# Optimization experiments

Measured on AMD Instinct MI355X. Metric: run time of the kernel, lower is better.

The kernel has to match this reference:

```python
import jax, jax.numpy as jnp
import numpy as np
from jax import lax

B, S, D, H, HFF, T = 256, 33, 42, 128, 256, 20
BN_EPS = 1e-5

def _bn(x, g, b):
    # eval-mode BatchNorm1d with running_mean=0, running_var=1
    return x * (g / jnp.sqrt(1.0 + BN_EPS)) + b

def _gelu(x):
    return jax.nn.gelu(x, approximate=False)  # torch default GELU (exact)

def setup_inputs() -> dict:
    key = jax.random.key(0)
    ks = iter(jax.random.split(key, 48))
    w = lambda shp, s=0.02: jax.random.normal(next(ks), shp, dtype=jnp.float32) * s
    z = lambda shp: jnp.zeros(shp, jnp.float32)
    o = lambda shp: jnp.ones(shp, jnp.float32)
    inp = {
        'interaction_path': jax.random.normal(next(ks), (B, S, D), dtype=jnp.float32),
        'timestamps': jnp.broadcast_to(jnp.arange(S, dtype=jnp.float32) * 0.1, (B, S)),
        # initial encoder: Linear(42->128), BN, GELU, Linear(128->128), BN
        'enc_w1': w((D, H)), 'enc_b1': z(H), 'enc_g1': o(H), 'enc_be1': z(H),
        'enc_w2': w((H, H)), 'enc_b2': z(H), 'enc_g2': o(H), 'enc_be2': z(H),
        # vector field: 128->256 (BN,GELU), 256->256 (BN,GELU) x2, 256->5376
        'vf_w0': w((H, HFF)), 'vf_b0': z(HFF), 'vf_g0': o(HFF), 'vf_be0': z(HFF),
        'vf_w1': w((HFF, HFF)), 'vf_b1': z(HFF), 'vf_g1': o(HFF), 'vf_be1': z(HFF),
        'vf_w2': w((HFF, HFF)), 'vf_b2': z(HFF), 'vf_g2': o(HFF), 'vf_be2': z(HFF),
        'vf_w3': w((HFF, H * D)), 'vf_b3': z(H * D),
        # multihead attention (seq_len = 1 -> softmax is identically 1)
        'wv': w((H, H)), 'bv': z(H), 'wo': w((H, H)), 'bo': z(H),
        # 20 trait decoders, stacked: 128->64->32->1
        'dw1': w((T, H, 64)), 'db1': z((T, 64)),
        'dw2': w((T, 64, 32)), 'db2': z((T, 32)),
        'dw3': w((T, 32, 1)), 'db3': z((T, 1)),
    }
    return inp

def reference(interaction_path, timestamps,
              enc_w1, enc_b1, enc_g1, enc_be1, enc_w2, enc_b2, enc_g2, enc_be2,
              vf_w0, vf_b0, vf_g0, vf_be0, vf_w1, vf_b1, vf_g1, vf_be1,
              vf_w2, vf_b2, vf_g2, vf_be2, vf_w3, vf_b3,
              wv, bv, wo, bo,
              dw1, db1, dw2, db2, dw3, db3):
    b = interaction_path.shape[0]
    # ---- initial encoder on X[:, 0] ----
    x0 = interaction_path[:, 0]                      # [B, D]
    h = _gelu(_bn(x0 @ enc_w1 + enc_b1, enc_g1, enc_be1))
    z0 = _bn(h @ enc_w2 + enc_b2, enc_g2, enc_be2)   # [B, H]

    # ---- CDE vector field: z -> [B, H, D] ----
    def vf(zz):
        y = _gelu(_bn(zz @ vf_w0 + vf_b0, vf_g0, vf_be0))
        y = _gelu(_bn(y @ vf_w1 + vf_b1, vf_g1, vf_be1))
        y = _gelu(_bn(y @ vf_w2 + vf_b2, vf_g2, vf_be2))
        return (y @ vf_w3 + vf_b3).reshape(b, H, D)

    def g(zz, dxdt):  # f(z) @ dX/dt  -> [B, H]
        return jnp.einsum('bhd,bd->bh', vf(zz), dxdt)

    # linear-interpolation control path: piecewise-constant derivative
    t = timestamps[0]                                # [S]
    dt = t[1:] - t[:-1]                              # [S-1]
    dX = interaction_path[:, 1:] - interaction_path[:, :-1]   # [B, S-1, D]
    dXdt = dX / dt[None, :, None]                    # [B, S-1, D]

    def step(zz, x):
        dxdt, hstep = x
        k1 = g(zz, dxdt)
        k2 = g(zz + 0.5 * hstep * k1, dxdt)
        k3 = g(zz + 0.5 * hstep * k2, dxdt)
        k4 = g(zz + hstep * k3, dxdt)
        return zz + (hstep / 6.0) * (k1 + 2.0 * k2 + 2.0 * k3 + k4), None

    zT, _ = lax.scan(step, z0, (jnp.swapaxes(dXdt, 0, 1), dt))  # [B, H]

    # ---- self-attention over a length-1 sequence: softmax==1 -> out_proj(v) ----
    attended = (zT @ wv + bv) @ wo + bo              # [B, H]

    # ---- 20 trait decoders (stacked / vectorized) ----
    h1 = _gelu(jnp.einsum('bh,thd->tbd', attended, dw1) + db1[:, None, :])
    h2 = _gelu(jnp.einsum('tbd,tde->tbe', h1, dw2) + db2[:, None, :])
    out = jax.nn.sigmoid(jnp.einsum('tbe,teo->tbo', h2, dw3) + db3[:, None, :])
    return jnp.transpose(out[..., 0], (1, 0))        # [B, 20]
```

## Files before the change

### kernel.cpp

```cpp
#include <hip/hip_runtime.h>
#include <cstdint>

constexpr int B    = 256;
constexpr int S    = 33;
constexpr int D    = 42;
constexpr int H    = 128;
constexpr int HFF  = 256;
constexpr int T    = 20;
constexpr int NSTEP = S - 1;
constexpr int DP   = D / 2;
constexpr int ADW  = 8192;
constexpr int CH   = 16;
constexpr int NCH  = NSTEP / CH;
#define BN_SCALE 0.9999950000374997f

typedef _Float16 h2v __attribute__((ext_vector_type(2)));
typedef _Float16 f16x8 __attribute__((ext_vector_type(8)));
typedef float    f32x4 __attribute__((ext_vector_type(4)));
union UH2 { uint32_t u; h2v h; };

__device__ __forceinline__ float fdot2u(uint32_t a, uint32_t b, float c) {
    UH2 x, y; x.u = a; y.u = b;
    return __builtin_amdgcn_fdot2(x.h, y.h, c, false);
}
__device__ __forceinline__ uint32_t packh2(float a, float b) {
    UH2 u; u.h = h2v{(_Float16)a, (_Float16)b}; return u.u;
}
__device__ __forceinline__ float gelu_exact(float x) {
    return 0.5f * x * (1.0f + erff(x * 0.70710678118654752f));
}
__device__ __forceinline__ float gelu_fast(float x) {
    float inner = x * (1.0f + 0.044715f * x * x);
    float E = __expf(1.5957691216f * inner);
    return x * E * __frcp_rn(E + 1.0f);
}
__device__ __forceinline__ int aswz(int idx) {
    return (idx & ~31) | ((idx & 31) ^ (((idx >> 9) & 3) << 1));
}

__global__ void pack_kernel(const float* __restrict__ w0, const float* __restrict__ w1,
                            const float* __restrict__ w2, const float* __restrict__ w3,
                            uint32_t* __restrict__ wcol, uint32_t* __restrict__ wp) {
    int idx = blockIdx.x * 256 + threadIdx.x;
    if (idx < 160 * 512) {
        int r = idx >> 9, t = idx & 511;
        int j = t >> 1, half = t & 1;
        float a, bb;
        if (r < 32)      { int ip = half * 32 + r;      a = w0[(2*ip)*HFF + j]; bb = w0[(2*ip+1)*HFF + j]; }
        else if (r < 96) { int ip = half * 64 + (r-32); a = w1[(2*ip)*HFF + j]; bb = w1[(2*ip+1)*HFF + j]; }
        else             { int ip = half * 64 + (r-96); a = w2[(2*ip)*HFF + j]; bb = w2[(2*ip+1)*HFF + j]; }
        wcol[idx] = packh2(a, bb);
    }
    if (idx < 32768 * 32) {
        int m = idx >> 5, dd = (idx & 31) * 2;
        int e = 4 * (m >> 9) + (m & 3);
        int h = (m >> 2) & 127;
        const float* row = w3 + (size_t)e * (H * D) + h * D;
        float a = (dd     < D) ? row[dd]     : 0.f;
        float b = (dd + 1 < D) ? row[dd + 1] : 0.f;
        wp[idx] = packh2(a, b);
    }
}

__global__ void prep_kernel(const float* __restrict__ path, const float* __restrict__ ts,
                            const float* __restrict__ ew1, const float* __restrict__ eb1,
                            const float* __restrict__ eg1, const float* __restrict__ ebe1,
                            const float* __restrict__ ew2, const float* __restrict__ eb2,
                            const float* __restrict__ eg2, const float* __restrict__ ebe2,
                            const float* __restrict__ b3,
                            float* __restrict__ zbuf, uint32_t* __restrict__ dxp,
                            float* __restrict__ bd3g, float* __restrict__ dtb) {
    __shared__ float x0[D], hb[H], dxs[NSTEP][D];
    int b = blockIdx.x, tid = threadIdx.x;
    if (tid < D) x0[tid] = path[b * S * D + tid];
    __syncthreads();
    {
        float acc = eb1[tid];
        for (int d = 0; d < D; ++d) acc += x0[d] * ew1[d * H + tid];
        hb[tid] = gelu_exact(acc * (eg1[tid] * BN_SCALE) + ebe1[tid]);
    }
    __syncthreads();
    {
        float acc = eb2[tid];
        for (int i = 0; i < H; ++i) acc += hb[i] * ew2[i * H + tid];
        zbuf[b * H + tid] = acc * (eg2[tid] * BN_SCALE) + ebe2[tid];
    }
    for (int idx = tid; idx < NSTEP * 32; idx += 128) {
        int s = idx >> 5, j2 = idx & 31;
        uint32_t val = 0;
        if (j2 < DP) {
            float dtv = ts[s + 1] - ts[s];
            int base = b * S * D + s * D + 2 * j2;
            float v0 = (path[base + D] - path[base]) / dtv;
            float v1 = (path[base + D + 1] - path[base + 1]) / dtv;
            dxs[s][2 * j2] = v0; dxs[s][2 * j2 + 1] = v1;
            val = packh2(v0, v1);
        }
        dxp[((size_t)(s * B + b)) * 32 + j2] = val;
    }
    __syncthreads();
    for (int s = 0; s < NSTEP; ++s) {
        float a = 0.f;
        for (int d = 0; d < D; ++d) a += b3[tid * D + d] * dxs[s][d];
        bd3g[(size_t)(s * B + b) * H + tid] = a;
    }
    if (b == 0 && tid < NSTEP) dtb[tid] = ts[tid + 1] - ts[tid];
}

__global__ void __launch_bounds__(256) amm_kernel(
    const uint32_t* __restrict__ wp, const uint32_t* __restrict__ dxp,
    uint32_t* __restrict__ Ach, int s0) {
    int t = threadIdx.x;
    int l = t & 63, wid = t >> 6;
    int mg = (blockIdx.x & 63) * 4 + wid;
    int sg = blockIdx.x >> 6;
    int lr = l & 15, lk = l >> 4;
    const char* wpB = (const char*)wp;
    const char* dxB = (const char*)dxp + (size_t)s0 * B * 128;
    char* asB = (char*)Ach;
    f16x8 af0[8], af1[8];
#pragma unroll
    for (int mi = 0; mi < 8; ++mi) {
        const f16x8* p = (const f16x8*)(wpB + ((size_t)(mg * 8 + mi) * 16 + lr) * 128 + lk * 16);
        af0[mi] = p[0]; af1[mi] = p[4];
    }
#pragma unroll
    for (int si = 0; si < 8; ++si) {
        int q = sg * 128 + si * 16 + lr;
        const f16x8* bp = (const f16x8*)(dxB + (size_t)q * 128 + lk * 16);
        f16x8 b0 = bp[0], b1 = bp[4];
        char* outB = asB + (size_t)q * 32768 + (mg * 128 + lk * 4);
#pragma unroll
        for (int mi = 0; mi < 8; ++mi) {
            f32x4 acc = {0.f, 0.f, 0.f, 0.f};
            acc = __builtin_amdgcn_mfma_f32_16x16x32_f16(af0[mi], b0, acc, 0, 0, 0);
            acc = __builtin_amdgcn_mfma_f32_16x16x32_f16(af1[mi], b1, acc, 0, 0, 0);
            uint32_t P0 = packh2(acc[0], acc[1]) + 0x00800080u;
            uint32_t P1 = packh2(acc[2], acc[3]) + 0x00800080u;
            uint32_t Q = __builtin_amdgcn_perm(P1, P0, 0x07050301u);
            *(uint32_t*)(outB + mi * 16) = Q;
        }
    }
}

__global__ void __launch_bounds__(512, 1)
__attribute__((amdgpu_waves_per_eu(2, 8)))
scan_kernel(
    const uint32_t* __restrict__ wcol, const uint32_t* __restrict__ Ach,
    const float* __restrict__ vb0, const float* __restrict__ vg0, const float* __restrict__ vbe0,
    const float* __restrict__ vb1, const float* __restrict__ vg1, const float* __restrict__ vbe1,
    const float* __restrict__ vb2, const float* __restrict__ vg2, const float* __restrict__ vbe2,
    const float* __restrict__ bd3g, const float* __restrict__ dtb,
    float* __restrict__ zbuf, int s0) {
    __shared__ __align__(16) uint32_t ABUF[2][ADW];
    __shared__ __align__(16) uint32_t zzPd[72];
    __shared__ __align__(16) uint32_t yA[136], yB[136], yC[136];
    int t = threadIdx.x, b = blockIdx.x;
    int j = t >> 1, half = t & 1;
    int h = t >> 2, g = t & 3;
    int hswz = h ^ (g << 3);
    uint32_t w0h[32], w1h[64], w2h[64];
#pragma unroll
    for (int r = 0; r < 32; ++r) w0h[r] = wcol[r * 512 + t];
#pragma unroll
    for (int r = 0; r < 64; ++r) w1h[r] = wcol[(32 + r) * 512 + t];
#pragma unroll
    for (int r = 0; r < 64; ++r) w2h[r] = wcol[(96 + r) * 512 + t];
    float c0s = vg0[j] * BN_SCALE, c0o = vb0[j] * c0s + vbe0[j];
    float c1s = vg1[j] * BN_SCALE, c1o = vb1[j] * c1s + vbe1[j];
    float c2s = vg2[j] * BN_SCALE, c2o = vb2[j] * c2s + vbe2[j];
    float zf = zbuf[b * H + h];
    {
        const uint4* Ag = (const uint4*)(Ach + (size_t)b * ADW);
        uint4 a0 = Ag[t], a1 = Ag[512 + t], a2 = Ag[1024 + t], a3 = Ag[1536 + t];
        uint4* Ad = (uint4*)ABUF[0];
        Ad[aswz(t)] = a0; Ad[aswz(512 + t)] = a1;
        Ad[aswz(1024 + t)] = a2; Ad[aswz(1536 + t)] = a3;
    }
    {
        float zhi = __shfl_down(zf, 4, 64);
        if ((t & 7) == 0) {
            int ip = t >> 3;
            zzPd[(ip >> 5) * 36 + (ip & 31)] = packh2(zf, zhi);
        }
    }
    __syncthreads();

    for (int sl = 0; sl < CH; ++sl) {
        int s = s0 + sl;
        float hstep = dtb[s];
        float bd3 = bd3g[(size_t)(s * B + b) * H + h];
        uint4 pf0, pf1, pf2, pf3;
        {
            int sn = (sl + 1 < CH) ? sl + 1 : sl;
            const uint4* Ag = (const uint4*)(Ach + (size_t)(sn * B + b) * ADW);
            pf0 = Ag[t]; pf1 = Ag[512 + t]; pf2 = Ag[1024 + t]; pf3 = Ag[1536 + t];
        }
        const uint32_t* AL = ABUF[sl & 1];
        float ksum = 0.f, kcur = 0.f;
        for (int r = 0; r < 4; ++r) {
            {
                float pa = 0.f, pb = 0.f, pc = 0.f, pd = 0.f;
                const uint4* zq = (const uint4*)(zzPd + half * 36);
#pragma unroll
                for (int u4 = 0; u4 < 8; ++u4) {
                    uint4 zv = zq[u4];
                    pa = fdot2u(w0h[4*u4+0], zv.x, pa); pb = fdot2u(w0h[4*u4+1], zv.y, pb);
                    pc = fdot2u(w0h[4*u4+2], zv.z, pc); pd = fdot2u(w0h[4*u4+3], zv.w, pd);
                }
                float p = (pa + pb) + (pc + pd);
                p += __shfl_xor(p, 1, 64);
                float v = gelu_fast(p * c0s + c0o);
                float vhi = __shfl_down(v, 2, 64);
                if ((t & 3) == 0) {
                    int ip = t >> 2;
                    yA[(ip >> 6) * 68 + (ip & 63)] = packh2(v, vhi);
                }
            }
            __syncthreads();
            {
                float pa = 0.f, pb = 0.f, pc = 0.f, pd = 0.f;
                const uint4* yq = (const uint4*)(yA + half * 68);
#pragma unroll
                for (int u4 = 0; u4 < 16; ++u4) {
                    uint4 yv = yq[u4];
                    pa = fdot2u(w1h[4*u4+0], yv.x, pa); pb = fdot2u(w1h[4*u4+1], yv.y, pb);
                    pc = fdot2u(w1h[4*u4+2], yv.z, pc); pd = fdot2u(w1h[4*u4+3], yv.w, pd);
                }
                float p = (pa + pb) + (pc + pd);
                p += __shfl_xor(p, 1, 64);
                float v = gelu_fast(p * c1s + c1o);
                float vhi = __shfl_down(v, 2, 64);
                if ((t & 3) == 0) {
                    int ip = t >> 2;
                    yB[(ip >> 6) * 68 + (ip & 63)] = packh2(v, vhi);
                }
            }
            __syncthreads();
            {
                float pa = 0.f, pb = 0.f, pc = 0.f, pd = 0.f;
                const uint4* yq = (const uint4*)(yB + half * 68);
#pragma unroll
                for (int u4 = 0; u4 < 16; ++u4) {
                    uint4 yv = yq[u4];
                    pa = fdot2u(w2h[4*u4+0], yv.x, pa); pb = fdot2u(w2h[4*u4+1], yv.y, pb);
                    pc = fdot2u(w2h[4*u4+2], yv.z, pc); pd = fdot2u(w2h[4*u4+3], yv.w, pd);
                }
                float p = (pa + pb) + (pc + pd);
                p += __shfl_xor(p, 1, 64);
                float v = gelu_fast(p * c2s + c2o);
                float vhi = __shfl_down(v, 2, 64);
                if ((t & 3) == 0) {
                    int ip = t >> 2;
                    yC[(ip >> 6) * 68 + (ip & 63)] = packh2(v, vhi);
                }
            }
            __syncthreads();
            {
                float pA = 0.f, pB = 0.f, pC = 0.f, pD = 0.f;
                int ybase = (g >> 1) * 68 + (g & 1) * 32;
                const uint4* yq = (const uint4*)(yC + ybase);
#pragma unroll
                for (int kk = 0; kk < 8; ++kk) {
                    uint4 yv = yq[kk];
                    int k0 = g * 16 + 2 * kk;
                    uint32_t Qa = AL[k0 * 128 + hswz];
                    uint32_t Qb = AL[(k0 + 1) * 128 + hswz];
                    pA = fdot2u(__builtin_amdgcn_perm(0u, Qa, 0x010C000Cu), yv.x, pA);
                    pB = fdot2u(__builtin_amdgcn_perm(0u, Qa, 0x030C020Cu), yv.y, pB);
                    pC = fdot2u(__builtin_amdgcn_perm(0u, Qb, 0x010C000Cu), yv.z, pC);
                    pD = fdot2u(__builtin_amdgcn_perm(0u, Qb, 0x030C020Cu), yv.w, pD);
                }
                float ptot = (pA + pB) + (pC + pD);
                ptot += __shfl_xor(ptot, 1, 64);
                ptot += __shfl_xor(ptot, 2, 64);
                kcur = bd3 + ptot;
                float wsm = (r == 1 || r == 2) ? 2.f : 1.f;
                ksum += wsm * kcur;
                float zz;
                if (r < 3) {
                    float cin = (r == 2) ? 1.f : 0.5f;
                    zz = zf + cin * hstep * kcur;
                } else {
                    zf += hstep * (1.f / 6.f) * ksum;
                    zz = zf;
                }
                float zhi = __shfl_down(zz, 4, 64);
                if ((t & 7) == 0) {
                    int ip = t >> 3;
                    zzPd[(ip >> 5) * 36 + (ip & 31)] = packh2(zz, zhi);
                }
            }
            if (r == 3) {
                uint4* Ad = (uint4*)ABUF[(sl + 1) & 1];
                Ad[aswz(t)] = pf0; Ad[aswz(512 + t)] = pf1;
                Ad[aswz(1024 + t)] = pf2; Ad[aswz(1536 + t)] = pf3;
            }
            __syncthreads();
        }
    }
    if ((t & 3) == 0) zbuf[b * H + h] = zf;
}

__global__ void att_kernel(const float* __restrict__ zbuf,
                           const float* __restrict__ wv, const float* __restrict__ bv,
                           const float* __restrict__ wo, const float* __restrict__ bo,
                           float* __restrict__ att) {
    __shared__ float zl[H], v[H];
    int b = blockIdx.x, tid = threadIdx.x;
    zl[tid] = zbuf[b * H + tid];
    __syncthreads();
    {
        float acc = bv[tid];
#pragma unroll 8
        for (int i = 0; i < H; ++i) acc += zl[i] * wv[i * H + tid];
        v[tid] = acc;
    }
    __syncthreads();
    {
        float acc = bo[tid];
#pragma unroll 8
        for (int i = 0; i < H; ++i) acc += v[i] * wo[i * H + tid];
        att[b * H + tid] = acc;
    }
}

__global__ void __launch_bounds__(64) dec_kernel(
    const float* __restrict__ att,
    const float* __restrict__ dw1, const float* __restrict__ db1,
    const float* __restrict__ dw2, const float* __restrict__ db2,
    const float* __restrict__ dw3, const float* __restrict__ db3,
    float* __restrict__ out) {
    int bid = blockIdx.x;
    int t = bid >> 8, b = bid & 255;
    int tid = threadIdx.x;
    __shared__ float al[H], h1l[64];
    al[tid] = att[b * H + tid];
    al[tid + 64] = att[b * H + tid + 64];
    __syncthreads();
    {
        float acc = db1[t * 64 + tid];
#pragma unroll 8
        for (int i = 0; i < H; ++i) acc += al[i] * dw1[t * H * 64 + i * 64 + tid];
        h1l[tid] = gelu_exact(acc);
    }
    __syncthreads();
    float v = 0.f;
    if (tid < 32) {
        float acc = db2[t * 32 + tid];
#pragma unroll 8
        for (int i = 0; i < 64; ++i) acc += h1l[i] * dw2[t * 64 * 32 + i * 32 + tid];
        v = gelu_exact(acc) * dw3[t * 32 + tid];
    }
#pragma unroll
    for (int off = 16; off >= 1; off >>= 1) v += __shfl_down(v, off, 64);
    if (tid == 0) out[b * T + t] = 1.f / (1.f + expf(-(v + db3[t])));
}

extern "C" void kernel_launch(void* const* d_in, const int* in_sizes, int n_in,
                              void* d_out, int out_size, void* d_ws, size_t ws_size,
                              hipStream_t stream) {
    const float* path = (const float*)d_in[0];
    const float* ts   = (const float*)d_in[1];
    const float* ew1  = (const float*)d_in[2];
    const float* eb1  = (const float*)d_in[3];
    const float* eg1  = (const float*)d_in[4];
    const float* ebe1 = (const float*)d_in[5];
    const float* ew2  = (const float*)d_in[6];
    const float* eb2  = (const float*)d_in[7];
    const float* eg2  = (const float*)d_in[8];
    const float* ebe2 = (const float*)d_in[9];
    const float* vw0  = (const float*)d_in[10];
    const float* vb0  = (const float*)d_in[11];
    const float* vg0  = (const float*)d_in[12];
    const float* vbe0 = (const float*)d_in[13];
    const float* vw1  = (const float*)d_in[14];
    const float* vb1  = (const float*)d_in[15];
    const float* vg1  = (const float*)d_in[16];
    const float* vbe1 = (const float*)d_in[17];
    const float* vw2  = (const float*)d_in[18];
    const float* vb2  = (const float*)d_in[19];
    const float* vg2  = (const float*)d_in[20];
    const float* vbe2 = (const float*)d_in[21];
    const float* vw3  = (const float*)d_in[22];
    const float* vb3  = (const float*)d_in[23];
    const float* wv   = (const float*)d_in[24];
    const float* bv   = (const float*)d_in[25];
    const float* wo   = (const float*)d_in[26];
    const float* bo   = (const float*)d_in[27];
    const float* dw1  = (const float*)d_in[28];
    const float* db1  = (const float*)d_in[29];
    const float* dw2  = (const float*)d_in[30];
    const float* db2  = (const float*)d_in[31];
    const float* dw3  = (const float*)d_in[32];
    const float* db3  = (const float*)d_in[33];

    char* ws = (char*)d_ws;
    size_t off = 0;
    auto take = [&](size_t bytes) { char* p = ws + off; off += (bytes + 255) & ~(size_t)255; return p; };
    uint32_t* Ach   = (uint32_t*)take((size_t)CH * B * ADW * 4);
    uint32_t* dxp   = (uint32_t*)take((size_t)NSTEP * B * 32 * 4);
    float*    bd3g  = (float*)take((size_t)NSTEP * B * H * 4);
    float*    dtb   = (float*)take(NSTEP * 4);
    float*    zbuf  = (float*)take((size_t)B * H * 4);
    float*    att   = (float*)take((size_t)B * H * 4);
    uint32_t* wcol  = (uint32_t*)take((size_t)160 * 512 * 4);
    uint32_t* wp    = (uint32_t*)take((size_t)32768 * 32 * 4);

    pack_kernel<<<(32768 * 32 + 255) / 256, 256, 0, stream>>>(vw0, vw1, vw2, vw3, wcol, wp);
    prep_kernel<<<B, 128, 0, stream>>>(path, ts, ew1, eb1, eg1, ebe1,
                                       ew2, eb2, eg2, ebe2, vb3, zbuf, dxp, bd3g, dtb);
    for (int c = 0; c < NCH; ++c) {
        amm_kernel<<<2048, 256, 0, stream>>>(wp, dxp, Ach, c * CH);
        scan_kernel<<<B, 512, 0, stream>>>(wcol, Ach,
                                           vb0, vg0, vbe0, vb1, vg1, vbe1, vb2, vg2, vbe2,
                                           bd3g, dtb, zbuf, c * CH);
    }
    att_kernel<<<B, 128, 0, stream>>>(zbuf, wv, bv, wo, bo, att);
    dec_kernel<<<T * B, 64, 0, stream>>>(att, dw1, db1, dw2, db2, dw3, db3, (float*)d_out);
}
```

Baseline: 620.6 us.

## Fuse next-chunk A-matrix GEMM into scan kernel with double-buffered chunks

The scan kernel now also launches extra blocks that compute the per-step A matrices for the next chunk, writing into a second buffer. This lets the MFMA-heavy GEMM run alongside the latency-bound scan, which only uses 256 blocks, instead of strictly alternating separate launches. The chunk size is halved to 8 so the two buffers fit, at the cost of more launches. Scan blocks raise their wave priority to protect the critical path, but the scan still competes with the GEMM blocks for bandwidth and CU resources.

Result: no change. 630.5 us (+1.6%).

```diff
diff --git a/kernel.cpp b/kernel.cpp
--- a/kernel.cpp
+++ b/kernel.cpp
@@ -10,7 +10,7 @@
 constexpr int NSTEP = S - 1;
 constexpr int DP   = D / 2;
 constexpr int ADW  = 8192;
-constexpr int CH   = 16;
+constexpr int CH   = 8;
 constexpr int NCH  = NSTEP / CH;
 #define BN_SCALE 0.9999950000374997f
 
@@ -145,17 +145,57 @@
 
 __global__ void __launch_bounds__(512, 1)
 __attribute__((amdgpu_waves_per_eu(2, 8)))
-scan_kernel(
-    const uint32_t* __restrict__ wcol, const uint32_t* __restrict__ Ach,
+fused_kernel(
+    const uint32_t* __restrict__ wcol, const uint32_t* __restrict__ AchR,
+    uint32_t* __restrict__ AchW,
+    const uint32_t* __restrict__ wp, const uint32_t* __restrict__ dxp,
     const float* __restrict__ vb0, const float* __restrict__ vg0, const float* __restrict__ vbe0,
     const float* __restrict__ vb1, const float* __restrict__ vg1, const float* __restrict__ vbe1,
     const float* __restrict__ vb2, const float* __restrict__ vg2, const float* __restrict__ vbe2,
     const float* __restrict__ bd3g, const float* __restrict__ dtb,
-    float* __restrict__ zbuf, int s0) {
+    float* __restrict__ zbuf, int s0_scan, int s0_amm) {
     __shared__ __align__(16) uint32_t ABUF[2][ADW];
     __shared__ __align__(16) uint32_t zzPd[72];
     __shared__ __align__(16) uint32_t yA[136], yB[136], yC[136];
-    int t = threadIdx.x, b = blockIdx.x;
+    int t = threadIdx.x;
+
+    if (blockIdx.x >= B) {
+        int rid = blockIdx.x - B;
+        int wid = t >> 6, l = t & 63;
+        int gw = rid * 8 + wid;
+        int mg = gw & 255, sg = gw >> 8;
+        int lr = l & 15, lk = l >> 4;
+        const char* wpB = (const char*)wp;
+        const char* dxB = (const char*)dxp + (size_t)s0_amm * B * 128;
+        char* asB = (char*)AchW;
+        f16x8 af0[8], af1[8];
+#pragma unroll
+        for (int mi = 0; mi < 8; ++mi) {
+            const f16x8* p = (const f16x8*)(wpB + ((size_t)(mg * 8 + mi) * 16 + lr) * 128 + lk * 16);
+            af0[mi] = p[0]; af1[mi] = p[4];
+        }
+#pragma unroll
+        for (int si = 0; si < 8; ++si) {
+            int q = sg * 128 + si * 16 + lr;
+            const f16x8* bp = (const f16x8*)(dxB + (size_t)q * 128 + lk * 16);
+            f16x8 b0 = bp[0], b1 = bp[4];
+            char* outB = asB + (size_t)q * 32768 + (mg * 128 + lk * 4);
+#pragma unroll
+            for (int mi = 0; mi < 8; ++mi) {
+                f32x4 acc = {0.f, 0.f, 0.f, 0.f};
+                acc = __builtin_amdgcn_mfma_f32_16x16x32_f16(af0[mi], b0, acc, 0, 0, 0);
+                acc = __builtin_amdgcn_mfma_f32_16x16x32_f16(af1[mi], b1, acc, 0, 0, 0);
+                uint32_t P0 = packh2(acc[0], acc[1]) + 0x00800080u;
+                uint32_t P1 = packh2(acc[2], acc[3]) + 0x00800080u;
+                uint32_t Q = __builtin_amdgcn_perm(P1, P0, 0x07050301u);
+                *(uint32_t*)(outB + mi * 16) = Q;
+            }
+        }
+        return;
+    }
+
+    __builtin_amdgcn_s_setprio(1);
+    int b = blockIdx.x;
     int j = t >> 1, half = t & 1;
     int h = t >> 2, g = t & 3;
     int hswz = h ^ (g << 3);
@@ -171,7 +211,7 @@
     float c2s = vg2[j] * BN_SCALE, c2o = vb2[j] * c2s + vbe2[j];
     float zf = zbuf[b * H + h];
     {
-        const uint4* Ag = (const uint4*)(Ach + (size_t)b * ADW);
+        const uint4* Ag = (const uint4*)(AchR + (size_t)b * ADW);
         uint4 a0 = Ag[t], a1 = Ag[512 + t], a2 = Ag[1024 + t], a3 = Ag[1536 + t];
         uint4* Ad = (uint4*)ABUF[0];
         Ad[aswz(t)] = a0; Ad[aswz(512 + t)] = a1;
@@ -187,13 +227,13 @@
     __syncthreads();
 
     for (int sl = 0; sl < CH; ++sl) {
-        int s = s0 + sl;
+        int s = s0_scan + sl;
         float hstep = dtb[s];
         float bd3 = bd3g[(size_t)(s * B + b) * H + h];
         uint4 pf0, pf1, pf2, pf3;
         {
             int sn = (sl + 1 < CH) ? sl + 1 : sl;
-            const uint4* Ag = (const uint4*)(Ach + (size_t)(sn * B + b) * ADW);
+            const uint4* Ag = (const uint4*)(AchR + (size_t)(sn * B + b) * ADW);
             pf0 = Ag[t]; pf1 = Ag[512 + t]; pf2 = Ag[1024 + t]; pf3 = Ag[1536 + t];
         }
         const uint32_t* AL = ABUF[sl & 1];
@@ -398,7 +438,8 @@
     char* ws = (char*)d_ws;
     size_t off = 0;
     auto take = [&](size_t bytes) { char* p = ws + off; off += (bytes + 255) & ~(size_t)255; return p; };
-    uint32_t* Ach   = (uint32_t*)take((size_t)CH * B * ADW * 4);
+    uint32_t* Ach0  = (uint32_t*)take((size_t)CH * B * ADW * 4);
+    uint32_t* Ach1  = (uint32_t*)take((size_t)CH * B * ADW * 4);
     uint32_t* dxp   = (uint32_t*)take((size_t)NSTEP * B * 32 * 4);
     float*    bd3g  = (float*)take((size_t)NSTEP * B * H * 4);
     float*    dtb   = (float*)take(NSTEP * 4);
@@ -406,15 +447,19 @@
     float*    att   = (float*)take((size_t)B * H * 4);
     uint32_t* wcol  = (uint32_t*)take((size_t)160 * 512 * 4);
     uint32_t* wp    = (uint32_t*)take((size_t)32768 * 32 * 4);
+    uint32_t* AchB[2] = { Ach0, Ach1 };
 
     pack_kernel<<<(32768 * 32 + 255) / 256, 256, 0, stream>>>(vw0, vw1, vw2, vw3, wcol, wp);
     prep_kernel<<<B, 128, 0, stream>>>(path, ts, ew1, eb1, eg1, ebe1,
                                        ew2, eb2, eg2, ebe2, vb3, zbuf, dxp, bd3g, dtb);
+    amm_kernel<<<1024, 256, 0, stream>>>(wp, dxp, AchB[0], 0);
     for (int c = 0; c < NCH; ++c) {
-        amm_kernel<<<2048, 256, 0, stream>>>(wp, dxp, Ach, c * CH);
-        scan_kernel<<<B, 512, 0, stream>>>(wcol, Ach,
-                                           vb0, vg0, vbe0, vb1, vg1, vbe1, vb2, vg2, vbe2,
-                                           bd3g, dtb, zbuf, c * CH);
+        int grid = (c < NCH - 1) ? (B + 512) : B;
+        int s_amm = (c < NCH - 1) ? (c + 1) * CH : 0;
+        fused_kernel<<<grid, 512, 0, stream>>>(
+            wcol, AchB[c & 1], AchB[(c + 1) & 1], wp, dxp,
+            vb0, vg0, vbe0, vb1, vg1, vbe1, vb2, vg2, vbe2,
+            bd3g, dtb, zbuf, c * CH, s_amm);
     }
     att_kernel<<<B, 128, 0, stream>>>(zbuf, wv, bv, wo, bo, att);
     dec_kernel<<<T * B, 64, 0, stream>>>(att, dw1, db1, dw2, db2, dw3, db3, (float*)d_out);
```
